# Performance work log

Measured on AMD Instinct MI355X. Metric: run time of the kernel, lower is better.

Reference implementation:

```python
import jax, jax.numpy as jnp
import numpy as np

EPS = 1e-12


def t5_layer_norm(x, w):
    # RMS norm without mean subtraction (T5 style)
    var = jnp.mean(x * x, axis=-1, keepdims=True)
    return w * (x * jax.lax.rsqrt(var + EPS))


def gether(h, a_simi, t_simi, adj):
    # h: [B,S,S,D]; a_simi/t_simi: [B,S]; adj: [B,S,S]
    diag = jnp.einsum('bssd->bsd', h)                 # h[b,l,l,:]
    h_adj = jnp.einsum('bld,blk->blkd', diag, adj)    # diag broadcast by adjacency
    h_y = h * t_simi[:, None, :, None]                # t_simi varies along axis 2
    h_x = h * a_simi[:, :, None, None]                # a_simi varies along axis 1
    h_left = jnp.pad(h_y, ((0, 0), (0, 0), (1, 0), (0, 0)))[:, :, :-1, :]
    h_right = jnp.pad(h_y, ((0, 0), (0, 0), (0, 1), (0, 0)))[:, :, 1:, :]
    h_up = jnp.pad(h_x, ((0, 0), (1, 0), (0, 0), (0, 0)))[:, :-1, :, :]
    h_down = jnp.pad(h_x, ((0, 0), (0, 1), (0, 0), (0, 0)))[:, 1:, :, :]
    return h + h_adj + h_left + h_right + h_up + h_down


def setup_inputs() -> dict:
    key = jax.random.key(0)
    ks = jax.random.split(key, 10)
    B, S, D_in, D_out = 8, 96, 768, 256
    table = jax.random.normal(ks[0], (B, S, S, D_in), dtype=jnp.float32)
    a_simi = jax.random.uniform(ks[1], (B, S), dtype=jnp.float32)
    t_simi = jax.random.uniform(ks[2], (B, S), dtype=jnp.float32)
    adj_matrix = jax.random.uniform(ks[3], (B, S, S), dtype=jnp.float32)
    s1 = 1.0 / np.sqrt(D_in)
    W1 = jax.random.uniform(ks[4], (D_in, D_in), jnp.float32, -s1, s1)
    b1 = jax.random.uniform(ks[5], (D_in,), jnp.float32, -s1, s1)
    g1 = jnp.ones((D_in,), jnp.float32)
    W2 = jax.random.uniform(ks[6], (D_in, D_out), jnp.float32, -s1, s1)
    b2 = jax.random.uniform(ks[7], (D_out,), jnp.float32, -s1, s1)
    g2 = jnp.ones((D_out,), jnp.float32)
    return {"table": table, "a_simi": a_simi, "t_simi": t_simi,
            "adj_matrix": adj_matrix, "W1": W1, "b1": b1, "g1": g1,
            "W2": W2, "b2": b2, "g2": g2}


def reference(table, a_simi, t_simi, adj_matrix, W1, b1, g1, W2, b2, g2):
    h0 = table
    h1 = gether(h0, a_simi, t_simi, adj_matrix)
    h1 = jax.nn.relu(t5_layer_norm((h1 + h0) @ W1 + b1, g1))
    h2 = gether(h1, a_simi, t_simi, adj_matrix)
    h2 = jax.nn.relu(t5_layer_norm((h2 + h1) @ W2 + b2, g2))
    return h2
```

## Files before the change

### kernel.cpp

```cpp
#include <hip/hip_runtime.h>

typedef __bf16 bf16;
typedef __bf16 bf16x4 __attribute__((ext_vector_type(4)));
typedef __bf16 bf16x8 __attribute__((ext_vector_type(8)));
typedef float f32x4 __attribute__((ext_vector_type(4)));
typedef float floatx4 __attribute__((ext_vector_type(4)));

#define S 96
#define DIN 768
#define DOUT 256
#define MROWS 73728

__device__ static inline void async16(const bf16* g, bf16* l) {
    __builtin_amdgcn_global_load_lds(
        (const __attribute__((address_space(1))) void*)g,
        (__attribute__((address_space(3))) void*)l,
        16, 0, 0);
}

__global__ __launch_bounds__(256) void k_gether1(
    const float* __restrict__ H, const float* __restrict__ Asim,
    const float* __restrict__ Tsim, const float* __restrict__ Adj,
    bf16* __restrict__ X)
{
    __shared__ float adjs[S];
    __shared__ float ts[S];
    __shared__ float diagf[DIN];
    int b = blockIdx.x / S, l = blockIdx.x % S;
    int tid = threadIdx.x;
    long row0 = (long)(b * S + l) * S;
    if (tid < S) {
        adjs[tid] = Adj[(b * S + l) * S + tid];
        ts[tid]   = Tsim[b * S + tid];
    }
    for (int i = tid; i < DIN / 4; i += 256)
        *(f32x4*)&diagf[i * 4] = *(const f32x4*)&H[(row0 + l) * DIN + i * 4];
    float a_up = (l > 0)     ? Asim[b * S + l - 1] : 0.f;
    float a_dn = (l < S - 1) ? Asim[b * S + l + 1] : 0.f;
    long du = (l > 0)     ? -(long)S * DIN : 0;
    long dd = (l < S - 1) ?  (long)S * DIN : 0;
    __syncthreads();

    for (int it = tid; it < S * (DIN / 4); it += 256) {
        int k = it / (DIN / 4);
        int c = it - k * (DIN / 4);
        const float* hc = H + (row0 + k) * DIN + c * 4;
        float tl = (k > 0)     ? ts[k - 1] : 0.f;
        float tr = (k < S - 1) ? ts[k + 1] : 0.f;
        long  dl = (k > 0)     ? -(long)DIN : 0;
        long  dr = (k < S - 1) ?  (long)DIN : 0;
        f32x4 vc = *(const f32x4*)hc;
        f32x4 vl = *(const f32x4*)(hc + dl);
        f32x4 vr = *(const f32x4*)(hc + dr);
        f32x4 vu = *(const f32x4*)(hc + du);
        f32x4 vd = *(const f32x4*)(hc + dd);
        float aj = adjs[k];
        bf16x4 o;
#pragma unroll
        for (int j = 0; j < 4; ++j) {
            float v = 2.f * vc[j] + aj * diagf[c * 4 + j]
                    + tl * vl[j] + tr * vr[j]
                    + a_up * vu[j] + a_dn * vd[j];
            o[j] = (bf16)v;
        }
        *(bf16x4*)&X[(row0 + k) * DIN + c * 4] = o;
    }
}

__global__ __launch_bounds__(256) void k_gether2(
    const bf16* __restrict__ Y, const float* __restrict__ INV,
    const float* __restrict__ G1, const float* __restrict__ Asim,
    const float* __restrict__ Tsim, const float* __restrict__ Adj,
    bf16* __restrict__ X)
{
    __shared__ float adjs[S];
    __shared__ float ts[S];
    __shared__ float diagf[DIN];
    __shared__ float g1s[DIN];
    int b = blockIdx.x / S, l = blockIdx.x % S;
    int tid = threadIdx.x;
    long row0 = (long)(b * S + l) * S;
    for (int i = tid; i < DIN; i += 256) g1s[i] = G1[i];
    __syncthreads();
    if (tid < S) {
        adjs[tid] = Adj[(b * S + l) * S + tid];
        ts[tid]   = Tsim[b * S + tid];
        float iv = INV[row0 + l];
        bf16x8 yv = *(const bf16x8*)&Y[(row0 + l) * DIN + tid * 8];
#pragma unroll
        for (int j = 0; j < 8; ++j) {
            float v = g1s[tid * 8 + j] * (float)yv[j] * iv;
            diagf[tid * 8 + j] = v > 0.f ? v : 0.f;
        }
    }
    float a_up = (l > 0)     ? Asim[b * S + l - 1] : 0.f;
    float a_dn = (l < S - 1) ? Asim[b * S + l + 1] : 0.f;
    long du = (l > 0)     ? -(long)S * DIN : 0;
    long dd = (l < S - 1) ?  (long)S * DIN : 0;
    int ou = (l > 0) ? -S : 0;
    int od = (l < S - 1) ? S : 0;
    __syncthreads();

    for (int it = tid; it < S * (DIN / 8); it += 256) {
        int k = it / (DIN / 8);
        int c = it - k * (DIN / 8);
        const bf16* yc = Y + (row0 + k) * DIN + c * 8;
        float tl = (k > 0)     ? ts[k - 1] : 0.f;
        float tr = (k < S - 1) ? ts[k + 1] : 0.f;
        int   ol = (k > 0)     ? -1 : 0;
        int   orr = (k < S - 1) ? 1 : 0;
        float ivc = INV[row0 + k];
        float ivl = INV[row0 + k + ol];
        float ivr = INV[row0 + k + orr];
        float ivu = INV[row0 + k + ou];
        float ivd = INV[row0 + k + od];
        bf16x8 vc = *(const bf16x8*)yc;
        bf16x8 vl = *(const bf16x8*)(yc + (long)ol * DIN);
        bf16x8 vr = *(const bf16x8*)(yc + (long)orr * DIN);
        bf16x8 vu = *(const bf16x8*)(yc + du);
        bf16x8 vd = *(const bf16x8*)(yc + dd);
        float aj = adjs[k];
        bf16x8 o;
#pragma unroll
        for (int j = 0; j < 8; ++j) {
            float g = g1s[c * 8 + j];
            float hc_ = g * (float)vc[j] * ivc; hc_ = hc_ > 0.f ? hc_ : 0.f;
            float hl_ = g * (float)vl[j] * ivl; hl_ = hl_ > 0.f ? hl_ : 0.f;
            float hr_ = g * (float)vr[j] * ivr; hr_ = hr_ > 0.f ? hr_ : 0.f;
            float hu_ = g * (float)vu[j] * ivu; hu_ = hu_ > 0.f ? hu_ : 0.f;
            float hd_ = g * (float)vd[j] * ivd; hd_ = hd_ > 0.f ? hd_ : 0.f;
            float v = 2.f * hc_ + aj * diagf[c * 8 + j]
                    + tl * hl_ + tr * hr_ + a_up * hu_ + a_dn * hd_;
            o[j] = (bf16)v;
        }
        *(bf16x8*)&X[(row0 + k) * DIN + c * 8] = o;
    }
}

__global__ __launch_bounds__(256) void k_gemm1(
    const bf16* __restrict__ Xm, const bf16* __restrict__ WT,
    const float* __restrict__ bias, bf16* __restrict__ Y,
    float* __restrict__ ssq)
{
    constexpr int K = 768, N = 768;
    __shared__ __align__(16) bf16 As[128 * 32];
    __shared__ __align__(16) bf16 Bs[192 * 32];
    int t = threadIdx.x;
    int rowBase = blockIdx.x * 128;
    int colBase = blockIdx.y * 192;
    int lane = t & 63, w = t >> 6;
    int quad = lane >> 4, l16 = lane & 15;
    int wr = w >> 1, wc = w & 1;

    floatx4 acc[4][6];
#pragma unroll
    for (int i = 0; i < 4; ++i)
#pragma unroll
        for (int j = 0; j < 6; ++j) acc[i][j] = (floatx4)0.f;

    int chunk = (t & 3) ^ ((t >> 3) & 3);
    const bf16* gA = Xm + (size_t)(rowBase + (t >> 2)) * K + chunk * 8;
    const bf16* gB = WT + (size_t)(colBase + (t >> 2)) * K + chunk * 8;
    bf16* ldsA = &As[t * 8];
    bf16* ldsB = &Bs[t * 8];

    for (int kk = 0; kk < K; kk += 32) {
        __syncthreads();
        async16(gA + kk, ldsA);
        async16(gA + kk + 64 * K, ldsA + 2048);
        async16(gB + kk, ldsB);
        async16(gB + kk + 64 * K, ldsB + 2048);
        async16(gB + kk + 128 * K, ldsB + 4096);
        __syncthreads();
        bf16x8 af[4], bfr[6];
#pragma unroll
        for (int i = 0; i < 4; ++i) {
            int ra = wr * 64 + i * 16 + l16;
            af[i] = *(const bf16x8*)&As[ra * 32 + (quad ^ ((ra >> 1) & 3)) * 8];
        }
#pragma unroll
        for (int j = 0; j < 6; ++j) {
            int rb = wc * 96 + j * 16 + l16;
            bfr[j] = *(const bf16x8*)&Bs[rb * 32 + (quad ^ ((rb >> 1) & 3)) * 8];
        }
#pragma unroll
        for (int i = 0; i < 4; ++i)
#pragma unroll
            for (int j = 0; j < 6; ++j)
                acc[i][j] = __builtin_amdgcn_mfma_f32_16x16x32_bf16(
                    af[i], bfr[j], acc[i][j], 0, 0, 0);
    }

    float bv[6];
#pragma unroll
    for (int j = 0; j < 6; ++j)
        bv[j] = bias[colBase + wc * 96 + j * 16 + l16];
#pragma unroll
    for (int i = 0; i < 4; ++i) {
#pragma unroll
        for (int r = 0; r < 4; ++r) {
            int row = rowBase + wr * 64 + i * 16 + quad * 4 + r;
            bf16* yp = Y + (size_t)row * N + colBase + wc * 96 + l16;
            float s = 0.f;
#pragma unroll
            for (int j = 0; j < 6; ++j) {
                float v = acc[i][j][r] + bv[j];
                s += v * v;
                yp[j * 16] = (bf16)v;
            }
            s += __shfl_xor(s, 1);
            s += __shfl_xor(s, 2);
            s += __shfl_xor(s, 4);
            s += __shfl_xor(s, 8);
            if (l16 == 0) atomicAdd(&ssq[row], s);
        }
    }
}

__global__ __launch_bounds__(256) void k_gemm2(
    const bf16* __restrict__ Xm, const bf16* __restrict__ WT,
    const float* __restrict__ bias, float* __restrict__ Y,
    float* __restrict__ ssq)
{
    constexpr int K = 768, N = 256;
    __shared__ __align__(16) bf16 As[128 * 32];
    __shared__ __align__(16) bf16 Bs[128 * 32];
    int t = threadIdx.x;
    int rowBase = blockIdx.x * 128;
    int colBase = blockIdx.y * 128;
    int lane = t & 63, w = t >> 6;
    int quad = lane >> 4, l16 = lane & 15;
    int wr = w >> 1, wc = w & 1;

    floatx4 acc[4][4];
#pragma unroll
    for (int i = 0; i < 4; ++i)
#pragma unroll
        for (int j = 0; j < 4; ++j) acc[i][j] = (floatx4)0.f;

    int chunk = (t & 3) ^ ((t >> 3) & 3);
    const bf16* gA = Xm + (size_t)(rowBase + (t >> 2)) * K + chunk * 8;
    const bf16* gB = WT + (size_t)(colBase + (t >> 2)) * K + chunk * 8;
    bf16* ldsA = &As[t * 8];
    bf16* ldsB = &Bs[t * 8];

    for (int kk = 0; kk < K; kk += 32) {
        __syncthreads();
        async16(gA + kk, ldsA);
        async16(gA + kk + 64 * K, ldsA + 2048);
        async16(gB + kk, ldsB);
        async16(gB + kk + 64 * K, ldsB + 2048);
        __syncthreads();
        bf16x8 af[4], bfr[4];
#pragma unroll
        for (int i = 0; i < 4; ++i) {
            int ra = wr * 64 + i * 16 + l16;
            af[i] = *(const bf16x8*)&As[ra * 32 + (quad ^ ((ra >> 1) & 3)) * 8];
        }
#pragma unroll
        for (int j = 0; j < 4; ++j) {
            int rb = wc * 64 + j * 16 + l16;
            bfr[j] = *(const bf16x8*)&Bs[rb * 32 + (quad ^ ((rb >> 1) & 3)) * 8];
        }
#pragma unroll
        for (int i = 0; i < 4; ++i)
#pragma unroll
            for (int j = 0; j < 4; ++j)
                acc[i][j] = __builtin_amdgcn_mfma_f32_16x16x32_bf16(
                    af[i], bfr[j], acc[i][j], 0, 0, 0);
    }

    float bv[4];
#pragma unroll
    for (int j = 0; j < 4; ++j)
        bv[j] = bias[colBase + wc * 64 + j * 16 + l16];
#pragma unroll
    for (int i = 0; i < 4; ++i) {
#pragma unroll
        for (int r = 0; r < 4; ++r) {
            int row = rowBase + wr * 64 + i * 16 + quad * 4 + r;
            float* yp = Y + (size_t)row * N + colBase + wc * 64 + l16;
            float s = 0.f;
#pragma unroll
            for (int j = 0; j < 4; ++j) {
                float v = acc[i][j][r] + bv[j];
                s += v * v;
                yp[j * 16] = v;
            }
            s += __shfl_xor(s, 1);
            s += __shfl_xor(s, 2);
            s += __shfl_xor(s, 4);
            s += __shfl_xor(s, 8);
            if (l16 == 0) atomicAdd(&ssq[row], s);
        }
    }
}

__global__ __launch_bounds__(256) void k_invr(float* ssq, int n, float invD)
{
    int i = blockIdx.x * 256 + threadIdx.x;
    if (i < n) ssq[i] = rsqrtf(ssq[i] * invD + 1e-12f);
}

__global__ __launch_bounds__(256) void k_final(
    const float* __restrict__ Y2, const float* __restrict__ ssq2,
    const float* __restrict__ G2, float* __restrict__ out)
{
    int gidx = blockIdx.x * 256 + threadIdx.x;
    int r = gidx >> 6;
    int c = (gidx & 63) * 4;
    float inv = rsqrtf(ssq2[r] * (1.f / DOUT) + 1e-12f);
    f32x4 yv = *(const f32x4*)&Y2[(size_t)r * DOUT + c];
    f32x4 o;
#pragma unroll
    for (int j = 0; j < 4; ++j) {
        float v = G2[c + j] * yv[j] * inv;
        o[j] = v > 0.f ? v : 0.f;
    }
    *(f32x4*)&out[(size_t)r * DOUT + c] = o;
}

__global__ __launch_bounds__(256) void k_castT(
    const float* __restrict__ in, bf16* __restrict__ out, int R, int C)
{
    __shared__ float tile[32][33];
    int lx = threadIdx.x & 31, ly = threadIdx.x >> 5;
    int c0 = blockIdx.x * 32, r0 = blockIdx.y * 32;
#pragma unroll
    for (int k = 0; k < 4; ++k)
        tile[ly + 8 * k][lx] = in[(size_t)(r0 + ly + 8 * k) * C + c0 + lx];
    __syncthreads();
#pragma unroll
    for (int k = 0; k < 4; ++k)
        out[(size_t)(c0 + ly + 8 * k) * R + r0 + lx] = (bf16)tile[lx][ly + 8 * k];
}

extern "C" void kernel_launch(void* const* d_in, const int* in_sizes, int n_in,
                              void* d_out, int out_size, void* d_ws, size_t ws_size,
                              hipStream_t stream)
{
    const float* table = (const float*)d_in[0];
    const float* asim  = (const float*)d_in[1];
    const float* tsim  = (const float*)d_in[2];
    const float* adj   = (const float*)d_in[3];
    const float* W1    = (const float*)d_in[4];
    const float* b1    = (const float*)d_in[5];
    const float* g1    = (const float*)d_in[6];
    const float* W2    = (const float*)d_in[7];
    const float* b2    = (const float*)d_in[8];
    const float* g2    = (const float*)d_in[9];
    float* out = (float*)d_out;

    char* ws = (char*)d_ws;
    const size_t SZ_X = (size_t)MROWS * DIN * 2;
    bf16*  X    = (bf16*)ws;
    bf16*  Y1   = (bf16*)(ws + SZ_X);
    float* Y2   = (float*)(ws + SZ_X);
    bf16*  W1T  = (bf16*)(ws + 2 * SZ_X);
    bf16*  W2T  = (bf16*)(ws + 2 * SZ_X + 1179648);
    float* ssq1 = (float*)(ws + 2 * SZ_X + 1179648 + 393216);
    float* ssq2 = ssq1 + MROWS;

    hipMemsetAsync(ssq1, 0, (size_t)MROWS * 4 * 2, stream);
    k_castT<<<dim3(DIN / 32, DIN / 32), 256, 0, stream>>>(W1, W1T, DIN, DIN);
    k_castT<<<dim3(DOUT / 32, DIN / 32), 256, 0, stream>>>(W2, W2T, DIN, DOUT);

    k_gether1<<<8 * S, 256, 0, stream>>>(table, asim, tsim, adj, X);
    k_gemm1<<<dim3(MROWS / 128, DIN / 192), 256, 0, stream>>>(X, W1T, b1, Y1, ssq1);
    k_invr<<<MROWS / 256, 256, 0, stream>>>(ssq1, MROWS, 1.f / DIN);
    k_gether2<<<8 * S, 256, 0, stream>>>(Y1, ssq1, g1, asim, tsim, adj, X);
    k_gemm2<<<dim3(MROWS / 128, DOUT / 128), 256, 0, stream>>>(X, W2T, b2, Y2, ssq2);
    k_final<<<(MROWS * DOUT / 4) / 256, 256, 0, stream>>>(Y2, ssq2, g2, out);
}
```

Baseline: 693.6 us.

## Fuse final RMS norm into GEMM2, retile GEMM1, split gether blocks by row halves

The second GEMM now computes all 256 output columns per block, reduces row sums of squares in shared memory, and applies the norm, gain and ReLU directly. This drops the fp32 Y2 intermediate, its atomics and the separate final kernel. GEMM1 switches to 128x128 tiles with a column-major block order so blocks sharing an X row tile run close together. Both gether kernels use a 2D grid where each block handles half the k rows, each wave takes one row and lanes stride columns, and gether2 moves from 8-wide to 4-wide bf16 loads. The trade is more register pressure in GEMM2 and smaller vector accesses in gether2.

```diff
diff --git a/kernel.cpp b/kernel.cpp
--- a/kernel.cpp
+++ b/kernel.cpp
@@ -41,29 +41,35 @@
     long dd = (l < S - 1) ?  (long)S * DIN : 0;
     __syncthreads();
 
-    for (int it = tid; it < S * (DIN / 4); it += 256) {
-        int k = it / (DIN / 4);
-        int c = it - k * (DIN / 4);
-        const float* hc = H + (row0 + k) * DIN + c * 4;
+    int lane = tid & 63, wv = tid >> 6;
+    int k0 = blockIdx.y * (S / 2);
+    for (int k = k0 + wv; k < k0 + S / 2; k += 4) {
         float tl = (k > 0)     ? ts[k - 1] : 0.f;
         float tr = (k < S - 1) ? ts[k + 1] : 0.f;
         long  dl = (k > 0)     ? -(long)DIN : 0;
         long  dr = (k < S - 1) ?  (long)DIN : 0;
-        f32x4 vc = *(const f32x4*)hc;
-        f32x4 vl = *(const f32x4*)(hc + dl);
-        f32x4 vr = *(const f32x4*)(hc + dr);
-        f32x4 vu = *(const f32x4*)(hc + du);
-        f32x4 vd = *(const f32x4*)(hc + dd);
         float aj = adjs[k];
-        bf16x4 o;
-#pragma unroll
-        for (int j = 0; j < 4; ++j) {
-            float v = 2.f * vc[j] + aj * diagf[c * 4 + j]
-                    + tl * vl[j] + tr * vr[j]
-                    + a_up * vu[j] + a_dn * vd[j];
-            o[j] = (bf16)v;
-        }
-        *(bf16x4*)&X[(row0 + k) * DIN + c * 4] = o;
+        const float* hrow = H + (row0 + k) * DIN;
+        bf16* xrow = X + (row0 + k) * DIN;
+#pragma unroll
+        for (int c = 0; c < 3; ++c) {
+            int col = (lane + c * 64) * 4;
+            const float* hc = hrow + col;
+            f32x4 vc = *(const f32x4*)hc;
+            f32x4 vl = *(const f32x4*)(hc + dl);
+            f32x4 vr = *(const f32x4*)(hc + dr);
+            f32x4 vu = *(const f32x4*)(hc + du);
+            f32x4 vd = *(const f32x4*)(hc + dd);
+            bf16x4 o;
+#pragma unroll
+            for (int j = 0; j < 4; ++j) {
+                float v = 2.f * vc[j] + aj * diagf[col + j]
+                        + tl * vl[j] + tr * vr[j]
+                        + a_up * vu[j] + a_dn * vd[j];
+                o[j] = (bf16)v;
+            }
+            *(bf16x4*)&xrow[col] = o;
+        }
     }
 }
 
@@ -101,39 +107,45 @@
     int od = (l < S - 1) ? S : 0;
     __syncthreads();
 
-    for (int it = tid; it < S * (DIN / 8); it += 256) {
-        int k = it / (DIN / 8);
-        int c = it - k * (DIN / 8);
-        const bf16* yc = Y + (row0 + k) * DIN + c * 8;
+    int lane = tid & 63, wv = tid >> 6;
+    int k0 = blockIdx.y * (S / 2);
+    for (int k = k0 + wv; k < k0 + S / 2; k += 4) {
         float tl = (k > 0)     ? ts[k - 1] : 0.f;
         float tr = (k < S - 1) ? ts[k + 1] : 0.f;
         int   ol = (k > 0)     ? -1 : 0;
         int   orr = (k < S - 1) ? 1 : 0;
+        float aj = adjs[k];
         float ivc = INV[row0 + k];
         float ivl = INV[row0 + k + ol];
         float ivr = INV[row0 + k + orr];
         float ivu = INV[row0 + k + ou];
         float ivd = INV[row0 + k + od];
-        bf16x8 vc = *(const bf16x8*)yc;
-        bf16x8 vl = *(const bf16x8*)(yc + (long)ol * DIN);
-        bf16x8 vr = *(const bf16x8*)(yc + (long)orr * DIN);
-        bf16x8 vu = *(const bf16x8*)(yc + du);
-        bf16x8 vd = *(const bf16x8*)(yc + dd);
-        float aj = adjs[k];
-        bf16x8 o;
-#pragma unroll
-        for (int j = 0; j < 8; ++j) {
-            float g = g1s[c * 8 + j];
-            float hc_ = g * (float)vc[j] * ivc; hc_ = hc_ > 0.f ? hc_ : 0.f;
-            float hl_ = g * (float)vl[j] * ivl; hl_ = hl_ > 0.f ? hl_ : 0.f;
-            float hr_ = g * (float)vr[j] * ivr; hr_ = hr_ > 0.f ? hr_ : 0.f;
-            float hu_ = g * (float)vu[j] * ivu; hu_ = hu_ > 0.f ? hu_ : 0.f;
-            float hd_ = g * (float)vd[j] * ivd; hd_ = hd_ > 0.f ? hd_ : 0.f;
-            float v = 2.f * hc_ + aj * diagf[c * 8 + j]
-                    + tl * hl_ + tr * hr_ + a_up * hu_ + a_dn * hd_;
-            o[j] = (bf16)v;
-        }
-        *(bf16x8*)&X[(row0 + k) * DIN + c * 8] = o;
+        const bf16* yrow = Y + (row0 + k) * DIN;
+        bf16* xrow = X + (row0 + k) * DIN;
+#pragma unroll
+        for (int c = 0; c < 3; ++c) {
+            int col = (lane + c * 64) * 4;
+            const bf16* yc = yrow + col;
+            bf16x4 vc = *(const bf16x4*)yc;
+            bf16x4 vl = *(const bf16x4*)(yc + (long)ol * DIN);
+            bf16x4 vr = *(const bf16x4*)(yc + (long)orr * DIN);
+            bf16x4 vu = *(const bf16x4*)(yc + du);
+            bf16x4 vd = *(const bf16x4*)(yc + dd);
+            bf16x4 o;
+#pragma unroll
+            for (int j = 0; j < 4; ++j) {
+                float g = g1s[col + j];
+                float hc_ = g * (float)vc[j] * ivc; hc_ = hc_ > 0.f ? hc_ : 0.f;
+                float hl_ = g * (float)vl[j] * ivl; hl_ = hl_ > 0.f ? hl_ : 0.f;
+                float hr_ = g * (float)vr[j] * ivr; hr_ = hr_ > 0.f ? hr_ : 0.f;
+                float hu_ = g * (float)vu[j] * ivu; hu_ = hu_ > 0.f ? hu_ : 0.f;
+                float hd_ = g * (float)vd[j] * ivd; hd_ = hd_ > 0.f ? hd_ : 0.f;
+                float v = 2.f * hc_ + aj * diagf[col + j]
+                        + tl * hl_ + tr * hr_ + a_up * hu_ + a_dn * hd_;
+                o[j] = (bf16)v;
+            }
+            *(bf16x4*)&xrow[col] = o;
+        }
     }
 }
 
@@ -144,90 +156,10 @@
 {
     constexpr int K = 768, N = 768;
     __shared__ __align__(16) bf16 As[128 * 32];
-    __shared__ __align__(16) bf16 Bs[192 * 32];
-    int t = threadIdx.x;
-    int rowBase = blockIdx.x * 128;
-    int colBase = blockIdx.y * 192;
-    int lane = t & 63, w = t >> 6;
-    int quad = lane >> 4, l16 = lane & 15;
-    int wr = w >> 1, wc = w & 1;
-
-    floatx4 acc[4][6];
-#pragma unroll
-    for (int i = 0; i < 4; ++i)
-#pragma unroll
-        for (int j = 0; j < 6; ++j) acc[i][j] = (floatx4)0.f;
-
-    int chunk = (t & 3) ^ ((t >> 3) & 3);
-    const bf16* gA = Xm + (size_t)(rowBase + (t >> 2)) * K + chunk * 8;
-    const bf16* gB = WT + (size_t)(colBase + (t >> 2)) * K + chunk * 8;
-    bf16* ldsA = &As[t * 8];
-    bf16* ldsB = &Bs[t * 8];
-
-    for (int kk = 0; kk < K; kk += 32) {
-        __syncthreads();
-        async16(gA + kk, ldsA);
-        async16(gA + kk + 64 * K, ldsA + 2048);
-        async16(gB + kk, ldsB);
-        async16(gB + kk + 64 * K, ldsB + 2048);
-        async16(gB + kk + 128 * K, ldsB + 4096);
-        __syncthreads();
-        bf16x8 af[4], bfr[6];
-#pragma unroll
-        for (int i = 0; i < 4; ++i) {
-            int ra = wr * 64 + i * 16 + l16;
-            af[i] = *(const bf16x8*)&As[ra * 32 + (quad ^ ((ra >> 1) & 3)) * 8];
-        }
-#pragma unroll
-        for (int j = 0; j < 6; ++j) {
-            int rb = wc * 96 + j * 16 + l16;
-            bfr[j] = *(const bf16x8*)&Bs[rb * 32 + (quad ^ ((rb >> 1) & 3)) * 8];
-        }
-#pragma unroll
-        for (int i = 0; i < 4; ++i)
-#pragma unroll
-            for (int j = 0; j < 6; ++j)
-                acc[i][j] = __builtin_amdgcn_mfma_f32_16x16x32_bf16(
-                    af[i], bfr[j], acc[i][j], 0, 0, 0);
-    }
-
-    float bv[6];
-#pragma unroll
-    for (int j = 0; j < 6; ++j)
-        bv[j] = bias[colBase + wc * 96 + j * 16 + l16];
-#pragma unroll
-    for (int i = 0; i < 4; ++i) {
-#pragma unroll
-        for (int r = 0; r < 4; ++r) {
-            int row = rowBase + wr * 64 + i * 16 + quad * 4 + r;
-            bf16* yp = Y + (size_t)row * N + colBase + wc * 96 + l16;
-            float s = 0.f;
-#pragma unroll
-            for (int j = 0; j < 6; ++j) {
-                float v = acc[i][j][r] + bv[j];
-                s += v * v;
-                yp[j * 16] = (bf16)v;
-            }
-            s += __shfl_xor(s, 1);
-            s += __shfl_xor(s, 2);
-            s += __shfl_xor(s, 4);
-            s += __shfl_xor(s, 8);
-            if (l16 == 0) atomicAdd(&ssq[row], s);
-        }
-    }
-}
-
-__global__ __launch_bounds__(256) void k_gemm2(
-    const bf16* __restrict__ Xm, const bf16* __restrict__ WT,
-    const float* __restrict__ bias, float* __restrict__ Y,
-    float* __restrict__ ssq)
-{
-    constexpr int K = 768, N = 256;
-    __shared__ __align__(16) bf16 As[128 * 32];
     __shared__ __align__(16) bf16 Bs[128 * 32];
     int t = threadIdx.x;
-    int rowBase = blockIdx.x * 128;
-    int colBase = blockIdx.y * 128;
+    int colBase = blockIdx.x * 128;
+    int rowBase = blockIdx.y * 128;
     int lane = t & 63, w = t >> 6;
     int quad = lane >> 4, l16 = lane & 15;
     int wr = w >> 1, wc = w & 1;
@@ -279,13 +211,13 @@
 #pragma unroll
         for (int r = 0; r < 4; ++r) {
             int row = rowBase + wr * 64 + i * 16 + quad * 4 + r;
-            float* yp = Y + (size_t)row * N + colBase + wc * 64 + l16;
+            bf16* yp = Y + (size_t)row * N + colBase + wc * 64 + l16;
             float s = 0.f;
 #pragma unroll
             for (int j = 0; j < 4; ++j) {
                 float v = acc[i][j][r] + bv[j];
                 s += v * v;
-                yp[j * 16] = v;
+                yp[j * 16] = (bf16)v;
             }
             s += __shfl_xor(s, 1);
             s += __shfl_xor(s, 2);
@@ -296,28 +228,107 @@
     }
 }
 
+__global__ __launch_bounds__(256, 2) void k_gemm2f(
+    const bf16* __restrict__ Xm, const bf16* __restrict__ WT,
+    const float* __restrict__ bias, const float* __restrict__ G2,
+    float* __restrict__ out)
+{
+    constexpr int K = 768, N = 256;
+    __shared__ __align__(16) bf16 As[128 * 32];
+    __shared__ __align__(16) bf16 Bs[256 * 32];
+    __shared__ float ssqs[2][128];
+    int t = threadIdx.x;
+    int rowBase = blockIdx.x * 128;
+    int lane = t & 63, w = t >> 6;
+    int quad = lane >> 4, l16 = lane & 15;
+    int wr = w >> 1, wc = w & 1;
+
+    floatx4 acc[4][8];
+#pragma unroll
+    for (int i = 0; i < 4; ++i)
+#pragma unroll
+        for (int j = 0; j < 8; ++j) acc[i][j] = (floatx4)0.f;
+
+    int chunk = (t & 3) ^ ((t >> 3) & 3);
+    const bf16* gA = Xm + (size_t)(rowBase + (t >> 2)) * K + chunk * 8;
+    const bf16* gB = WT + (size_t)(t >> 2) * K + chunk * 8;
+    bf16* ldsA = &As[t * 8];
+    bf16* ldsB = &Bs[t * 8];
+
+    for (int kk = 0; kk < K; kk += 32) {
+        __syncthreads();
+        async16(gA + kk, ldsA);
+        async16(gA + kk + 64 * K, ldsA + 2048);
+        async16(gB + kk, ldsB);
+        async16(gB + kk + 64 * K, ldsB + 2048);
+        async16(gB + kk + 128 * K, ldsB + 4096);
+        async16(gB + kk + 192 * K, ldsB + 6144);
+        __syncthreads();
+        bf16x8 af[4], bfr[8];
+#pragma unroll
+        for (int i = 0; i < 4; ++i) {
+            int ra = wr * 64 + i * 16 + l16;
+            af[i] = *(const bf16x8*)&As[ra * 32 + (quad ^ ((ra >> 1) & 3)) * 8];
+        }
+#pragma unroll
+        for (int j = 0; j < 8; ++j) {
+            int rb = wc * 128 + j * 16 + l16;
+            bfr[j] = *(const bf16x8*)&Bs[rb * 32 + (quad ^ ((rb >> 1) & 3)) * 8];
+        }
+#pragma unroll
+        for (int i = 0; i < 4; ++i)
+#pragma unroll
+            for (int j = 0; j < 8; ++j)
+                acc[i][j] = __builtin_amdgcn_mfma_f32_16x16x32_bf16(
+                    af[i], bfr[j], acc[i][j], 0, 0, 0);
+    }
+
+    float bv[8], gv[8];
+#pragma unroll
+    for (int j = 0; j < 8; ++j) {
+        int col = wc * 128 + j * 16 + l16;
+        bv[j] = bias[col];
+        gv[j] = G2[col];
+    }
+#pragma unroll
+    for (int i = 0; i < 4; ++i) {
+#pragma unroll
+        for (int r = 0; r < 4; ++r) {
+            float s = 0.f;
+#pragma unroll
+            for (int j = 0; j < 8; ++j) {
+                float v = acc[i][j][r] + bv[j];
+                s += v * v;
+            }
+            s += __shfl_xor(s, 1);
+            s += __shfl_xor(s, 2);
+            s += __shfl_xor(s, 4);
+            s += __shfl_xor(s, 8);
+            if (l16 == 0)
+                ssqs[wc][wr * 64 + i * 16 + quad * 4 + r] = s;
+        }
+    }
+    __syncthreads();
+#pragma unroll
+    for (int i = 0; i < 4; ++i) {
+#pragma unroll
+        for (int r = 0; r < 4; ++r) {
+            int lr = wr * 64 + i * 16 + quad * 4 + r;
+            float inv = rsqrtf((ssqs[0][lr] + ssqs[1][lr]) * (1.f / N) + 1e-12f);
+            float* op = out + (size_t)(rowBase + lr) * N + wc * 128 + l16;
+#pragma unroll
+            for (int j = 0; j < 8; ++j) {
+                float v = (acc[i][j][r] + bv[j]) * gv[j] * inv;
+                op[j * 16] = v > 0.f ? v : 0.f;
+            }
+        }
+    }
+}
+
 __global__ __launch_bounds__(256) void k_invr(float* ssq, int n, float invD)
 {
     int i = blockIdx.x * 256 + threadIdx.x;
     if (i < n) ssq[i] = rsqrtf(ssq[i] * invD + 1e-12f);
-}
-
-__global__ __launch_bounds__(256) void k_final(
-    const float* __restrict__ Y2, const float* __restrict__ ssq2,
-    const float* __restrict__ G2, float* __restrict__ out)
-{
-    int gidx = blockIdx.x * 256 + threadIdx.x;
-    int r = gidx >> 6;
-    int c = (gidx & 63) * 4;
-    float inv = rsqrtf(ssq2[r] * (1.f / DOUT) + 1e-12f);
-    f32x4 yv = *(const f32x4*)&Y2[(size_t)r * DOUT + c];
-    f32x4 o;
-#pragma unroll
-    for (int j = 0; j < 4; ++j) {
-        float v = G2[c + j] * yv[j] * inv;
-        o[j] = v > 0.f ? v : 0.f;
-    }
-    *(f32x4*)&out[(size_t)r * DOUT + c] = o;
 }
 
 __global__ __launch_bounds__(256) void k_castT(
@@ -355,20 +366,17 @@
     const size_t SZ_X = (size_t)MROWS * DIN * 2;
     bf16*  X    = (bf16*)ws;
     bf16*  Y1   = (bf16*)(ws + SZ_X);
-    float* Y2   = (float*)(ws + SZ_X);
     bf16*  W1T  = (bf16*)(ws + 2 * SZ_X);
     bf16*  W2T  = (bf16*)(ws + 2 * SZ_X + 1179648);
     float* ssq1 = (float*)(ws + 2 * SZ_X + 1179648 + 393216);
-    float* ssq2 = ssq1 + MROWS;
-
-    hipMemsetAsync(ssq1, 0, (size_t)MROWS * 4 * 2, stream);
+
+    hipMemsetAsync(ssq1, 0, (size_t)MROWS * 4, stream);
     k_castT<<<dim3(DIN / 32, DIN / 32), 256, 0, stream>>>(W1, W1T, DIN, DIN);
     k_castT<<<dim3(DOUT / 32, DIN / 32), 256, 0, stream>>>(W2, W2T, DIN, DOUT);
 
-    k_gether1<<<8 * S, 256, 0, stream>>>(table, asim, tsim, adj, X);
-    k_gemm1<<<dim3(MROWS / 128, DIN / 192), 256, 0, stream>>>(X, W1T, b1, Y1, ssq1);
+    k_gether1<<<dim3(8 * S, 2), 256, 0, stream>>>(table, asim, tsim, adj, X);
+    k_gemm1<<<dim3(DIN / 128, MROWS / 128), 256, 0, stream>>>(X, W1T, b1, Y1, ssq1);
     k_invr<<<MROWS / 256, 256, 0, stream>>>(ssq1, MROWS, 1.f / DIN);
-    k_gether2<<<8 * S, 256, 0, stream>>>(Y1, ssq1, g1, asim, tsim, adj, X);
-    k_gemm2<<<dim3(MROWS / 128, DOUT / 128), 256, 0, stream>>>(X, W2T, b2, Y2, ssq2);
-    k_final<<<(MROWS * DOUT / 4) / 256, 256, 0, stream>>>(Y2, ssq2, g2, out);
-}
+    k_gether2<<<dim3(8 * S, 2), 256, 0, stream>>>(Y1, ssq1, g1, asim, tsim, adj, X);
+    k_gemm2f<<<MROWS / 128, 256, 0, stream>>>(X, W2T, b2, g2, out);
+}
```

Result: no change. 682.1 us (-1.7%).
